# Kernel tuning notes

Hardware: AMD Instinct MI355X
Metric: run time of the kernel (lower is better)

## Reference

```python
import jax, jax.numpy as jnp
import numpy as np
from jax import lax

BN_EPS = 1e-5
C = 256


def _conv_bn_relu(x, w, gamma, beta, mean, var):
    # x: [B,C,H,W], w: [C,C,3,3]; VALID conv, stride 1, then inference BN + ReLU
    y = lax.conv_general_dilated(x, w, window_strides=(1, 1), padding='VALID',
                                 dimension_numbers=('NCHW', 'OIHW', 'NCHW'))
    scale = gamma * lax.rsqrt(var + BN_EPS)
    shift = beta - mean * scale
    y = y * scale[None, :, None, None] + shift[None, :, None, None]
    return jax.nn.relu(y)


def _xcorr_depthwise(search, kernel):
    # search: [B,C,Hs,Ws], kernel: [B,C,Hk,Wk]
    # per-(batch, channel) valid cross-correlation (groups = B*C in torch)
    c = search.shape[1]

    def one(s, k):  # s: [C,Hs,Ws], k: [C,Hk,Wk]
        return lax.conv_general_dilated(
            s[None], k[:, None], window_strides=(1, 1), padding='VALID',
            dimension_numbers=('NCHW', 'OIHW', 'NCHW'),
            feature_group_count=c)[0]

    return jax.vmap(one)(search, kernel)  # [B,C,Ho,Wo]


def setup_inputs() -> dict:
    key = jax.random.key(0)
    ks = jax.random.split(key, 8)
    B = 128
    kernel = jax.random.normal(ks[0], (B, C, 7, 7), dtype=jnp.float32)
    search = jax.random.normal(ks[1], (B, C, 31, 31), dtype=jnp.float32)
    std = np.sqrt(2.0 / (3 * 3 * C)).astype(np.float32)
    w_kernel = jax.random.normal(ks[2], (C, C, 3, 3), dtype=jnp.float32) * std
    w_search = jax.random.normal(ks[3], (C, C, 3, 3), dtype=jnp.float32) * std
    bn_k_gamma = jnp.ones((C,), jnp.float32)
    bn_k_beta = jnp.zeros((C,), jnp.float32)
    bn_k_mean = jax.random.normal(ks[4], (C,), dtype=jnp.float32) * 0.1
    bn_k_var = jax.random.uniform(ks[5], (C,), dtype=jnp.float32, minval=0.5, maxval=1.5)
    bn_s_gamma = jnp.ones((C,), jnp.float32)
    bn_s_beta = jnp.zeros((C,), jnp.float32)
    bn_s_mean = jax.random.normal(ks[6], (C,), dtype=jnp.float32) * 0.1
    bn_s_var = jax.random.uniform(ks[7], (C,), dtype=jnp.float32, minval=0.5, maxval=1.5)
    return dict(kernel=kernel, search=search,
                w_kernel=w_kernel, bn_k_gamma=bn_k_gamma, bn_k_beta=bn_k_beta,
                bn_k_mean=bn_k_mean, bn_k_var=bn_k_var,
                w_search=w_search, bn_s_gamma=bn_s_gamma, bn_s_beta=bn_s_beta,
                bn_s_mean=bn_s_mean, bn_s_var=bn_s_var)


def reference(kernel, search, w_kernel, bn_k_gamma, bn_k_beta, bn_k_mean, bn_k_var,
              w_search, bn_s_gamma, bn_s_beta, bn_s_mean, bn_s_var):
    k = _conv_bn_relu(kernel, w_kernel, bn_k_gamma, bn_k_beta, bn_k_mean, bn_k_var)  # [B,C,5,5]
    s = _conv_bn_relu(search, w_search, bn_s_gamma, bn_s_beta, bn_s_mean, bn_s_var)  # [B,C,29,29]
    return _xcorr_depthwise(s, k)  # [B,C,25,25]
```

## Files before the change

### kernel.cpp

```cpp
#include <hip/hip_runtime.h>
#include <hip/hip_bf16.h>

#define BN_EPS 1e-5f
constexpr int C = 256;

typedef __attribute__((ext_vector_type(8))) short bf16x8;
typedef __attribute__((ext_vector_type(4))) float f32x4;

static __device__ __forceinline__ unsigned short f2bf(float f) {
    __hip_bfloat16 h = __float2bfloat16(f);
    return *reinterpret_cast<unsigned short*>(&h);
}
static __device__ __forceinline__ float bf2f(unsigned short u) {
    unsigned int v = ((unsigned int)u) << 16;
    return __uint_as_float(v);
}

__global__ __launch_bounds__(256) void prep_fused(
    const float* __restrict__ wk, const float* __restrict__ bkg, const float* __restrict__ bkv,
    unsigned short* __restrict__ wkt,
    const float* __restrict__ ws, const float* __restrict__ bsg, const float* __restrict__ bsv,
    unsigned short* __restrict__ wst,
    const float* __restrict__ kin, unsigned short* __restrict__ ipk,
    int nw)
{
    __shared__ float s_t[64][65];
    const int bid = blockIdx.x;
    const int t = threadIdx.x;

    if (bid < nw) {
        const bool isk = bid < (nw >> 1);
        const int n = isk ? bid : bid - (nw >> 1);
        const float* w = isk ? wk : ws;
        const float* g = isk ? bkg : bsg;
        const float* v = isk ? bkv : bsv;
        unsigned short* wt = isk ? wkt : wst;
        const float scale = g[n] * rsqrtf(v[n] + BN_EPS);
        const float* wp = w + ((size_t)n * C + t) * 9;
#pragma unroll
        for (int k = 0; k < 9; ++k)
            wt[((size_t)k * C + n) * C + t] = f2bf(wp[k] * scale);
        return;
    }

    const int idx = bid - nw;
    const int b = idx >> 2, c0 = (idx & 3) * 64;
    constexpr int HW = 49;
    const float* ip = kin + ((size_t)b * C + c0) * HW;

#pragma unroll
    for (int it = 0; it < 4; ++it) {
        int i = t + it * 256;
        int cl = i >> 4, q = i & 15;
#pragma unroll
        for (int j = 0; j < 4; ++j) {
            int p = q * 4 + j;
            s_t[cl][p] = (p < HW) ? ip[(size_t)cl * HW + p] : 0.f;
        }
    }
    __syncthreads();

    unsigned short* op = ipk + (size_t)b * HW * C + c0;
#pragma unroll
    for (int it = 0; it < 2; ++it) {
        int i = t + it * 256;
        int pl = i >> 3, gq = i & 7;
        if (pl < HW) {
            bf16x8 pk;
#pragma unroll
            for (int u = 0; u < 8; ++u)
                pk[u] = (short)f2bf(s_t[gq * 8 + u][pl]);
            *(bf16x8*)&op[(size_t)pl * C + gq * 8] = pk;
        }
    }
}

__global__ __launch_bounds__(256) void l2_fused(
    const float* __restrict__ sin_, unsigned short* __restrict__ ips,
    const unsigned short* __restrict__ ipk, const unsigned short* __restrict__ wkt,
    const float* __restrict__ bkg, const float* __restrict__ bkb,
    const float* __restrict__ bkm, const float* __restrict__ bkv,
    float* __restrict__ kbuf, int nkc)
{
    __shared__ __align__(16) char smem[16640];
    const int bid = blockIdx.x;
    const int t = threadIdx.x;

    if (bid < nkc) {
        constexpr int WIN = 7, HW = 49, WOUT = 5, NPOS = 25;
        constexpr int BPB = 2, PPB = 32, MF = 2, NF = 2;
        constexpr int APIX = 49, LDK = 40;
        constexpr int SLOTS_B = APIX * 4, SLOTS = BPB * SLOTS_B;
        constexpr int ITERS = 2;

        short* s_a = (short*)smem;

        const int lane = t & 63, wave = t >> 6;
        const int wm = wave >> 1, wn = wave & 1;
        const int lr = lane >> 4, lc = lane & 15;

        const int n0 = (bid & 3) * 64;
        const int b0 = (bid >> 2) * 2;

        int arow[MF];
#pragma unroll
        for (int m = 0; m < MF; ++m) {
            int pm = wm * 32 + m * 16 + lc;
            int bb = pm / PPB;
            int p = pm % PPB;
            p = p < NPOS ? p : NPOS - 1;
            int y = p / WOUT, x = p % WOUT;
            arow[m] = (bb * APIX + y * WIN + x) * LDK;
        }

        f32x4 acc[MF][NF];
#pragma unroll
        for (int m = 0; m < MF; ++m)
#pragma unroll
            for (int n = 0; n < NF; ++n) acc[m][n] = f32x4{0.f, 0.f, 0.f, 0.f};

        int sbb[ITERS], spx[ITERS], ssl[ITERS];
#pragma unroll
        for (int it = 0; it < ITERS; ++it) {
            int i = t + it * 256;
            int ii = i < SLOTS ? i : 0;
            int bb = ii / SLOTS_B;
            int r = ii - bb * SLOTS_B;
            sbb[it] = bb; spx[it] = r >> 2; ssl[it] = r & 3;
        }

        const unsigned short* wb = wkt + (size_t)(n0 + wn * 32 + lc) * C + lr * 8;

#define K_LOAD(c0_)                                                            \
        _Pragma("unroll")                                                      \
        for (int it = 0; it < ITERS; ++it) {                                   \
            const unsigned short* sp =                                         \
                ipk + ((size_t)(b0 + sbb[it]) * HW + spx[it]) * C + (c0_) + ssl[it] * 8; \
            stg[it] = *(const bf16x8*)sp;                                      \
        }
#define K_WRITE()                                                              \
        _Pragma("unroll")                                                      \
        for (int it = 0; it < ITERS; ++it)                                     \
            *(bf16x8*)&s_a[(sbb[it] * APIX + spx[it]) * LDK + ssl[it] * 8] = stg[it];

        {
            bf16x8 stg[ITERS];
            K_LOAD(0)
            K_WRITE()
        }

#pragma unroll 1
        for (int ch = 0; ch < 8; ++ch) {
            const int c0 = ch * 32;
            __syncthreads();

            bf16x8 stg[ITERS];
            if (ch < 7) { K_LOAD(c0 + 32) }

            bf16x8 bcur[NF], bnxt[NF];
#pragma unroll
            for (int n = 0; n < NF; ++n)
                bnxt[n] = *(const bf16x8*)&wb[(size_t)0 * (C * C) + n * (16 * C) + c0];

#pragma unroll
            for (int tap = 0; tap < 9; ++tap) {
                const int dy = tap / 3, dx = tap % 3;
#pragma unroll
                for (int n = 0; n < NF; ++n) bcur[n] = bnxt[n];
                if (tap < 8) {
#pragma unroll
                    for (int n = 0; n < NF; ++n)
                        bnxt[n] = *(const bf16x8*)&wb[(size_t)(tap + 1) * (C * C) + n * (16 * C) + c0];
                }
                bf16x8 af[MF];
#pragma unroll
                for (int m = 0; m < MF; ++m)
                    af[m] = *(const bf16x8*)&s_a[arow[m] + (dy * WIN + dx) * LDK + lr * 8];
#pragma unroll
                for (int m = 0; m < MF; ++m)
#pragma unroll
                    for (int n = 0; n < NF; ++n)
                        acc[m][n] = __builtin_amdgcn_mfma_f32_16x16x32_bf16(
                            af[m], bcur[n], acc[m][n], 0, 0, 0);
            }

            __syncthreads();
            if (ch < 7) { K_WRITE() }
        }
#undef K_LOAD
#undef K_WRITE

#pragma unroll
        for (int n = 0; n < NF; ++n) {
            const int co = n0 + wn * 32 + n * 16 + lc;
            const float sc = bkg[co] * rsqrtf(bkv[co] + BN_EPS);
            const float bias = bkb[co] - bkm[co] * sc;
#pragma unroll
            for (int m = 0; m < MF; ++m) {
                int pm = wm * 32 + m * 16 + lr * 4;
                int bb = pm / PPB;
                int p = pm % PPB;
                int b = b0 + bb;
                f32x4 v = acc[m][n];
                float rr[4] = {fmaxf(v.x + bias, 0.f), fmaxf(v.y + bias, 0.f),
                               fmaxf(v.z + bias, 0.f), fmaxf(v.w + bias, 0.f)};
                float* op = kbuf + ((size_t)b * C + co) * 28 + p;
#pragma unroll
                for (int i = 0; i < 4; ++i)
                    if (p + i < NPOS) op[i] = rr[i];
            }
        }
        return;
    }

    {
        constexpr int HW = 961;
        float (*s_t)[65] = (float(*)[65])smem;
        const int idx = bid - nkc;
        const int px0 = (idx & 15) * 64;
        const int c0 = ((idx >> 4) & 3) * 64;
        const int b = idx >> 6;
        const float* ip = sin_ + ((size_t)b * C + c0) * HW;

#pragma unroll
        for (int it = 0; it < 4; ++it) {
            int i = t + it * 256;
            int cl = i >> 4, q = i & 15;
#pragma unroll
            for (int j = 0; j < 4; ++j) {
                int p = px0 + q * 4 + j;
                s_t[cl][q * 4 + j] = (p < HW) ? ip[(size_t)cl * HW + p] : 0.f;
            }
        }
        __syncthreads();

        unsigned short* op = ips + (size_t)b * HW * C + (size_t)px0 * C + c0;
#pragma unroll
        for (int it = 0; it < 2; ++it) {
            int i = t + it * 256;
            int pl = i >> 3, gq = i & 7;
            if (px0 + pl < HW) {
                bf16x8 pk;
#pragma unroll
                for (int u = 0; u < 8; ++u)
                    pk[u] = (short)f2bf(s_t[gq * 8 + u][pl]);
                *(bf16x8*)&op[(size_t)pl * C + gq * 8] = pk;
            }
        }
    }
}

__global__ __launch_bounds__(512, 2) void sconv_mfma(
    const unsigned short* __restrict__ in,
    const unsigned short* __restrict__ wt,
    const float* __restrict__ gamma, const float* __restrict__ beta,
    const float* __restrict__ mean, const float* __restrict__ var,
    unsigned short* __restrict__ outp)
{
    constexpr int WOUT = 29, NPOS = 841;
    constexpr int BM = 224, MF = 7, NF = 4;
    constexpr int LDK = 36;
    constexpr int ROWS = 11;
    constexpr int APIX = ROWS * 31;
    constexpr int ABUF = APIX * LDK;
    constexpr int BBUF = 256 * LDK;
    constexpr int AIT = 3;
    constexpr int BIT = 2;

    __shared__ __align__(16) short s_a[2 * ABUF];
    __shared__ __align__(16) short s_b[4 * BBUF];

    const int t = threadIdx.x;
    const int lane = t & 63, wave = t >> 6;
    const int wm = wave >> 2, wn = wave & 3;
    const int lr = lane >> 4, lc = lane & 15;

    const int p0 = blockIdx.x * BM;
    const int b  = blockIdx.y;
    const int y0 = p0 / WOUT;
    const int R  = min(ROWS, 31 - y0);
    const int npix = R * 31;

    const unsigned short* in_b = in + (size_t)b * (961 * 256);

    int arow[MF];
#pragma unroll
    for (int m = 0; m < MF; ++m) {
        int pm = wm * 112 + m * 16 + lc;
        int p = p0 + pm; p = p < NPOS ? p : NPOS - 1;
        int y = p / WOUT, x = p - y * WOUT;
        arow[m] = ((y - y0) * 31 + x) * LDK + lr * 8;
    }

    const unsigned short* aptr[AIT]; int aoff[AIT];
#pragma unroll
    for (int it = 0; it < AIT; ++it) {
        int i = t + it * 512;
        int px = i >> 2, sl = i & 3;
        px = px < npix ? px : 0;
        aptr[it] = in_b + (size_t)(y0 * 31 + px) * 256 + sl * 8;
        aoff[it] = px * LDK + sl * 8;
    }
    const unsigned short* bptr[BIT]; int boff[BIT];
#pragma unroll
    for (int it = 0; it < BIT; ++it) {
        int i = t + it * 512;
        int n = i >> 2, sl = i & 3;
        bptr[it] = wt + (size_t)n * 256 + sl * 8;
        boff[it] = n * LDK + sl * 8;
    }

    f32x4 acc[MF][NF];
#pragma unroll
    for (int m = 0; m < MF; ++m)
#pragma unroll
        for (int n = 0; n < NF; ++n) acc[m][n] = f32x4{0.f, 0.f, 0.f, 0.f};

    bf16x8 bstg0[BIT], bstg1[BIT], astg[AIT];

#pragma unroll
    for (int it = 0; it < BIT; ++it) bstg0[it] = *(const bf16x8*)(bptr[it]);
#pragma unroll
    for (int it = 0; it < BIT; ++it) bstg1[it] = *(const bf16x8*)(bptr[it] + 65536);
#pragma unroll
    for (int it = 0; it < AIT; ++it) astg[it] = *(const bf16x8*)(aptr[it]);
#pragma unroll
    for (int it = 0; it < BIT; ++it) *(bf16x8*)&s_b[boff[it]] = bstg0[it];
#pragma unroll
    for (int it = 0; it < BIT; ++it) *(bf16x8*)&s_b[BBUF + boff[it]] = bstg1[it];
#pragma unroll
    for (int it = 0; it < AIT; ++it) *(bf16x8*)&s_a[aoff[it]] = astg[it];
    __syncthreads();

#define READ_FRAGS(S, AF, BF)                                                  \
    {                                                                          \
        const int tap_ = (S) % 9;                                              \
        const int dt_ = (tap_ / 3) * 31 + (tap_ % 3);                          \
        const int ab_ = (((S) / 9) & 1) * ABUF;                                \
        const int bb_ = ((S) & 3) * BBUF;                                      \
        _Pragma("unroll")                                                      \
        for (int n = 0; n < NF; ++n)                                           \
            BF[n] = *(const bf16x8*)&s_b[bb_ + (wn * 64 + n * 16 + lc) * LDK + lr * 8]; \
        _Pragma("unroll")                                                      \
        for (int m = 0; m < MF; ++m)                                           \
            AF[m] = *(const bf16x8*)&s_a[ab_ + arow[m] + dt_ * LDK];           \
    }

#define MFMA_STEP(AF, BF)                                                      \
    _Pragma("unroll")                                                          \
    for (int m = 0; m < MF; ++m)                                               \
        _Pragma("unroll")                                                      \
        for (int n = 0; n < NF; ++n)                                           \
            acc[m][n] = __builtin_amdgcn_mfma_f32_16x16x32_bf16(               \
                AF[m], BF[n], acc[m][n], 0, 0, 0);

#pragma unroll 1
    for (int pr = 0; pr < 35; ++pr) {
        const int s0 = 2 * pr, s1 = s0 + 1;

        {
            const int cb = (s0 % 9 == 0) ? s0 / 9 : ((s1 % 9 == 0) ? s1 / 9 : -1);
            if (cb >= 0 && cb < 7) {
                const int co_ = (cb + 1) * 32;
#pragma unroll
                for (int it = 0; it < AIT; ++it)
                    astg[it] = *(const bf16x8*)(aptr[it] + co_);
            }
        }

        bf16x8 af0[MF], bf0[NF], af1[MF], bf1[NF];
        READ_FRAGS(s0, af0, bf0)
        READ_FRAGS(s1, af1, bf1)

        MFMA_STEP(af0, bf0)

        {
            const int u0 = s0 + 2, u1 = s1 + 2;
            const int t0 = u0 % 9, c0_ = (u0 / 9) * 32;
            const int t1 = u1 % 9, c1_ = (u1 / 9) * 32;
#pragma unroll
            for (int it = 0; it < BIT; ++it)
                bstg0[it] = *(const bf16x8*)(bptr[it] + (size_t)t0 * 65536 + c0_);
#pragma unroll
            for (int it = 0; it < BIT; ++it)
                bstg1[it] = *(const bf16x8*)(bptr[it] + (size_t)t1 * 65536 + c1_);
        }

        MFMA_STEP(af1, bf1)

        {
            const int w0 = ((s0 + 2) & 3) * BBUF, w1 = ((s1 + 2) & 3) * BBUF;
#pragma unroll
            for (int it = 0; it < BIT; ++it)
                *(bf16x8*)&s_b[w0 + boff[it]] = bstg0[it];
#pragma unroll
            for (int it = 0; it < BIT; ++it)
                *(bf16x8*)&s_b[w1 + boff[it]] = bstg1[it];
        }

        __builtin_amdgcn_sched_group_barrier(0x100, 11, 0);
#pragma unroll
        for (int q = 0; q < 5; ++q) {
            __builtin_amdgcn_sched_group_barrier(0x008, 3, 0);
            __builtin_amdgcn_sched_group_barrier(0x100, 1, 0);
        }
#pragma unroll
        for (int q = 0; q < 6; ++q) {
            __builtin_amdgcn_sched_group_barrier(0x008, 2, 0);
            __builtin_amdgcn_sched_group_barrier(0x100, 1, 0);
        }
        __builtin_amdgcn_sched_group_barrier(0x008, 1, 0);
        __builtin_amdgcn_sched_group_barrier(0x020, 4, 0);
        __builtin_amdgcn_sched_group_barrier(0x008, 28, 0);
        __builtin_amdgcn_sched_group_barrier(0x200, 4, 0);

        {
            const int cw = (s0 % 9 == 7) ? s0 / 9 : ((s1 % 9 == 7) ? s1 / 9 : -1);
            if (cw >= 0 && cw < 7) {
                const int dst = ((cw & 1) ^ 1) * ABUF;
#pragma unroll
                for (int it = 0; it < AIT; ++it)
                    *(bf16x8*)&s_a[dst + aoff[it]] = astg[it];
            }
        }
        __syncthreads();
    }

    {
        bf16x8 af0[MF], bf0[NF], af1[MF], bf1[NF];
        READ_FRAGS(70, af0, bf0)
        READ_FRAGS(71, af1, bf1)
        MFMA_STEP(af0, bf0)
        MFMA_STEP(af1, bf1)
    }
#undef READ_FRAGS
#undef MFMA_STEP

#pragma unroll
    for (int n = 0; n < NF; ++n) {
        const int co = wn * 64 + n * 16 + lc;
        const float sc = gamma[co] * rsqrtf(var[co] + BN_EPS);
        const float bias = beta[co] - mean[co] * sc;
#pragma unroll
        for (int m = 0; m < MF; ++m) {
            int pm = wm * 112 + m * 16 + lr * 4;
            int p = p0 + pm;
            f32x4 v = acc[m][n];
            float r0 = fmaxf(v.x + bias, 0.f);
            float r1 = fmaxf(v.y + bias, 0.f);
            float r2 = fmaxf(v.z + bias, 0.f);
            float r3 = fmaxf(v.w + bias, 0.f);
            unsigned short* op = outp + ((size_t)b * C + co) * 844 + p;
            if (p + 4 <= NPOS) {
                ushort4 pk;
                pk.x = f2bf(r0); pk.y = f2bf(r1); pk.z = f2bf(r2); pk.w = f2bf(r3);
                *(ushort4*)op = pk;
            } else {
                float rr[4] = {r0, r1, r2, r3};
#pragma unroll
                for (int i = 0; i < 4; ++i)
                    if (p + i < NPOS) op[i] = f2bf(rr[i]);
            }
        }
    }
}

__global__ __launch_bounds__(256) void xcorr_dw(
    const unsigned short* __restrict__ s, const float* __restrict__ k,
    float* __restrict__ out)
{
    const int bc0 = blockIdx.x * 2;
    const int t = threadIdx.x;

    __shared__ float s_s[2][844];
    __shared__ float s_k[2][25];

#pragma unroll
    for (int it = 0; it < 2; ++it) {
        int i = t + it * 256;
        if (i < 422) {
            int pl = i < 211 ? 0 : 1;
            int q = i - pl * 211;
            ushort4 v = *(const ushort4*)(s + (size_t)(bc0 + pl) * 844 + 4 * q);
            s_s[pl][4 * q + 0] = bf2f(v.x);
            s_s[pl][4 * q + 1] = bf2f(v.y);
            s_s[pl][4 * q + 2] = bf2f(v.z);
            s_s[pl][4 * q + 3] = bf2f(v.w);
        }
    }
    if (t < 50) s_k[t / 25][t % 25] = k[(size_t)(bc0 + t / 25) * 28 + t % 25];
    __syncthreads();

    if (t >= 250) return;
    const int ch = t / 125;
    const int r = t - ch * 125;
    const int y = r / 5;
    const int xb = (r - y * 5) * 5;

    float kk[25];
#pragma unroll
    for (int i = 0; i < 25; ++i) kk[i] = s_k[ch][i];

    float w[5][9];
#pragma unroll
    for (int dy = 0; dy < 5; ++dy)
#pragma unroll
        for (int dx = 0; dx < 9; ++dx)
            w[dy][dx] = s_s[ch][(y + dy) * 29 + xb + dx];

    float o[5] = {0.f, 0.f, 0.f, 0.f, 0.f};
#pragma unroll
    for (int dy = 0; dy < 5; ++dy)
#pragma unroll
        for (int dx = 0; dx < 5; ++dx) {
            const float kv = kk[dy * 5 + dx];
#pragma unroll
            for (int oo = 0; oo < 5; ++oo)
                o[oo] += w[dy][oo + dx] * kv;
        }

    float* op = out + (size_t)(bc0 + ch) * 625 + y * 25 + xb;
#pragma unroll
    for (int oo = 0; oo < 5; ++oo) op[oo] = o[oo];
}

extern "C" void kernel_launch(void* const* d_in, const int* in_sizes, int n_in,
                              void* d_out, int out_size, void* d_ws, size_t ws_size,
                              hipStream_t stream) {
    const float* kin = (const float*)d_in[0];
    const float* sin_ = (const float*)d_in[1];
    const float* wk = (const float*)d_in[2];
    const float* bkg = (const float*)d_in[3];
    const float* bkb = (const float*)d_in[4];
    const float* bkm = (const float*)d_in[5];
    const float* bkv = (const float*)d_in[6];
    const float* ws_ = (const float*)d_in[7];
    const float* bsg = (const float*)d_in[8];
    const float* bsb = (const float*)d_in[9];
    const float* bsm = (const float*)d_in[10];
    const float* bsv = (const float*)d_in[11];
    float* out = (float*)d_out;

    char* base = (char*)d_ws;
    unsigned short* wkt = (unsigned short*)base;
    unsigned short* wst = wkt + (size_t)9 * C * C;
    char* gbase = base + 2359296;

    const size_t perb_is = (size_t)961 * C * 2;
    const size_t perb_ik = (size_t)49 * C * 2;
    const size_t perb_sb = (size_t)844 * C * 2;
    const size_t perb_kb = (size_t)28 * C * 4;
    const size_t perb = perb_is + perb_ik + perb_sb + perb_kb;

    int G = (int)((ws_size - 2359296) / perb);
    if (G > 128) G = 128;
    G &= ~1;
    if (G < 2) G = 2;

    unsigned short* ips  = (unsigned short*)gbase;
    unsigned short* ipk  = (unsigned short*)(gbase + (size_t)G * perb_is);
    unsigned short* sbuf = (unsigned short*)(gbase + (size_t)G * (perb_is + perb_ik));
    float*          kbuf = (float*)(gbase + (size_t)G * (perb_is + perb_ik + perb_sb));

    for (int g0 = 0; g0 < 128; g0 += G) {
        const int g = (128 - g0) < G ? (128 - g0) : G;
        const int nw = (g0 == 0) ? 512 : 0;

        prep_fused<<<nw + 4 * g, 256, 0, stream>>>(
            wk, bkg, bkv, wkt, ws_, bsg, bsv, wst,
            kin + (size_t)g0 * C * 49, ipk, nw);

        const int nkc = 2 * g;
        l2_fused<<<nkc + 64 * g, 256, 0, stream>>>(
            sin_ + (size_t)g0 * C * 961, ips, ipk, wkt,
            bkg, bkb, bkm, bkv, kbuf, nkc);

        sconv_mfma<<<dim3(4, g), 512, 0, stream>>>(
            ips, wst, bsg, bsb, bsm, bsv, sbuf);

        xcorr_dw<<<(unsigned)g * (C / 2), 256, 0, stream>>>(
            sbuf, kbuf, out + (size_t)g0 * C * 625);
    }
}
```

Measured before the change: 262.2 us.

## Fuse input transpose into conv kernels and merge both convs into one launch

Removes the separate NCHW-to-NHWC bf16 transpose passes for the search and template inputs. The conv kernels now read fp32 NCHW directly, pack pairs of channels to bf16 and write them into shared memory. Both 3x3 convs go into a single mega_conv launch with block ranges split by blockIdx, and the per-group batching loop and the manual sched_group_barrier ordering are dropped. This saves a full round trip of the transposed intermediates through global memory and several launches. In exchange, the global loads inside the main MFMA loop are strided 4-byte scalar reads instead of 16-byte vectors, and the hand-tuned instruction interleaving is lost.

```diff
diff --git a/kernel.cpp b/kernel.cpp
--- a/kernel.cpp
+++ b/kernel.cpp
@@ -15,247 +15,41 @@
     unsigned int v = ((unsigned int)u) << 16;
     return __uint_as_float(v);
 }
-
-__global__ __launch_bounds__(256) void prep_fused(
+static __device__ __forceinline__ unsigned int pack_bf2(float a, float b) {
+    return (unsigned int)f2bf(a) | ((unsigned int)f2bf(b) << 16);
+}
+
+__global__ __launch_bounds__(256) void wprep_both(
     const float* __restrict__ wk, const float* __restrict__ bkg, const float* __restrict__ bkv,
     unsigned short* __restrict__ wkt,
     const float* __restrict__ ws, const float* __restrict__ bsg, const float* __restrict__ bsv,
-    unsigned short* __restrict__ wst,
-    const float* __restrict__ kin, unsigned short* __restrict__ ipk,
-    int nw)
+    unsigned short* __restrict__ wst)
 {
-    __shared__ float s_t[64][65];
-    const int bid = blockIdx.x;
-    const int t = threadIdx.x;
-
-    if (bid < nw) {
-        const bool isk = bid < (nw >> 1);
-        const int n = isk ? bid : bid - (nw >> 1);
-        const float* w = isk ? wk : ws;
-        const float* g = isk ? bkg : bsg;
-        const float* v = isk ? bkv : bsv;
-        unsigned short* wt = isk ? wkt : wst;
-        const float scale = g[n] * rsqrtf(v[n] + BN_EPS);
-        const float* wp = w + ((size_t)n * C + t) * 9;
-#pragma unroll
-        for (int k = 0; k < 9; ++k)
-            wt[((size_t)k * C + n) * C + t] = f2bf(wp[k] * scale);
-        return;
-    }
-
-    const int idx = bid - nw;
-    const int b = idx >> 2, c0 = (idx & 3) * 64;
-    constexpr int HW = 49;
-    const float* ip = kin + ((size_t)b * C + c0) * HW;
-
-#pragma unroll
-    for (int it = 0; it < 4; ++it) {
-        int i = t + it * 256;
-        int cl = i >> 4, q = i & 15;
-#pragma unroll
-        for (int j = 0; j < 4; ++j) {
-            int p = q * 4 + j;
-            s_t[cl][p] = (p < HW) ? ip[(size_t)cl * HW + p] : 0.f;
-        }
-    }
-    __syncthreads();
-
-    unsigned short* op = ipk + (size_t)b * HW * C + c0;
-#pragma unroll
-    for (int it = 0; it < 2; ++it) {
-        int i = t + it * 256;
-        int pl = i >> 3, gq = i & 7;
-        if (pl < HW) {
-            bf16x8 pk;
-#pragma unroll
-            for (int u = 0; u < 8; ++u)
-                pk[u] = (short)f2bf(s_t[gq * 8 + u][pl]);
-            *(bf16x8*)&op[(size_t)pl * C + gq * 8] = pk;
-        }
-    }
-}
-
-__global__ __launch_bounds__(256) void l2_fused(
-    const float* __restrict__ sin_, unsigned short* __restrict__ ips,
-    const unsigned short* __restrict__ ipk, const unsigned short* __restrict__ wkt,
+    const int bid = blockIdx.x, t = threadIdx.x;
+    const bool isk = bid < 256;
+    const int n = isk ? bid : bid - 256;
+    const float* w = isk ? wk : ws;
+    const float* g = isk ? bkg : bsg;
+    const float* v = isk ? bkv : bsv;
+    unsigned short* wt = isk ? wkt : wst;
+    const float scale = g[n] * rsqrtf(v[n] + BN_EPS);
+    const float* wp = w + ((size_t)n * C + t) * 9;
+#pragma unroll
+    for (int k = 0; k < 9; ++k)
+        wt[((size_t)k * C + n) * C + t] = f2bf(wp[k] * scale);
+}
+
+__global__ __launch_bounds__(512, 2) void mega_conv(
+    const float* __restrict__ sin_,
+    const float* __restrict__ kin,
+    const unsigned short* __restrict__ wst,
+    const unsigned short* __restrict__ wkt,
+    const float* __restrict__ bsg, const float* __restrict__ bsb,
+    const float* __restrict__ bsm, const float* __restrict__ bsv,
     const float* __restrict__ bkg, const float* __restrict__ bkb,
     const float* __restrict__ bkm, const float* __restrict__ bkv,
-    float* __restrict__ kbuf, int nkc)
-{
-    __shared__ __align__(16) char smem[16640];
-    const int bid = blockIdx.x;
-    const int t = threadIdx.x;
-
-    if (bid < nkc) {
-        constexpr int WIN = 7, HW = 49, WOUT = 5, NPOS = 25;
-        constexpr int BPB = 2, PPB = 32, MF = 2, NF = 2;
-        constexpr int APIX = 49, LDK = 40;
-        constexpr int SLOTS_B = APIX * 4, SLOTS = BPB * SLOTS_B;
-        constexpr int ITERS = 2;
-
-        short* s_a = (short*)smem;
-
-        const int lane = t & 63, wave = t >> 6;
-        const int wm = wave >> 1, wn = wave & 1;
-        const int lr = lane >> 4, lc = lane & 15;
-
-        const int n0 = (bid & 3) * 64;
-        const int b0 = (bid >> 2) * 2;
-
-        int arow[MF];
-#pragma unroll
-        for (int m = 0; m < MF; ++m) {
-            int pm = wm * 32 + m * 16 + lc;
-            int bb = pm / PPB;
-            int p = pm % PPB;
-            p = p < NPOS ? p : NPOS - 1;
-            int y = p / WOUT, x = p % WOUT;
-            arow[m] = (bb * APIX + y * WIN + x) * LDK;
-        }
-
-        f32x4 acc[MF][NF];
-#pragma unroll
-        for (int m = 0; m < MF; ++m)
-#pragma unroll
-            for (int n = 0; n < NF; ++n) acc[m][n] = f32x4{0.f, 0.f, 0.f, 0.f};
-
-        int sbb[ITERS], spx[ITERS], ssl[ITERS];
-#pragma unroll
-        for (int it = 0; it < ITERS; ++it) {
-            int i = t + it * 256;
-            int ii = i < SLOTS ? i : 0;
-            int bb = ii / SLOTS_B;
-            int r = ii - bb * SLOTS_B;
-            sbb[it] = bb; spx[it] = r >> 2; ssl[it] = r & 3;
-        }
-
-        const unsigned short* wb = wkt + (size_t)(n0 + wn * 32 + lc) * C + lr * 8;
-
-#define K_LOAD(c0_)                                                            \
-        _Pragma("unroll")                                                      \
-        for (int it = 0; it < ITERS; ++it) {                                   \
-            const unsigned short* sp =                                         \
-                ipk + ((size_t)(b0 + sbb[it]) * HW + spx[it]) * C + (c0_) + ssl[it] * 8; \
-            stg[it] = *(const bf16x8*)sp;                                      \
-        }
-#define K_WRITE()                                                              \
-        _Pragma("unroll")                                                      \
-        for (int it = 0; it < ITERS; ++it)                                     \
-            *(bf16x8*)&s_a[(sbb[it] * APIX + spx[it]) * LDK + ssl[it] * 8] = stg[it];
-
-        {
-            bf16x8 stg[ITERS];
-            K_LOAD(0)
-            K_WRITE()
-        }
-
-#pragma unroll 1
-        for (int ch = 0; ch < 8; ++ch) {
-            const int c0 = ch * 32;
-            __syncthreads();
-
-            bf16x8 stg[ITERS];
-            if (ch < 7) { K_LOAD(c0 + 32) }
-
-            bf16x8 bcur[NF], bnxt[NF];
-#pragma unroll
-            for (int n = 0; n < NF; ++n)
-                bnxt[n] = *(const bf16x8*)&wb[(size_t)0 * (C * C) + n * (16 * C) + c0];
-
-#pragma unroll
-            for (int tap = 0; tap < 9; ++tap) {
-                const int dy = tap / 3, dx = tap % 3;
-#pragma unroll
-                for (int n = 0; n < NF; ++n) bcur[n] = bnxt[n];
-                if (tap < 8) {
-#pragma unroll
-                    for (int n = 0; n < NF; ++n)
-                        bnxt[n] = *(const bf16x8*)&wb[(size_t)(tap + 1) * (C * C) + n * (16 * C) + c0];
-                }
-                bf16x8 af[MF];
-#pragma unroll
-                for (int m = 0; m < MF; ++m)
-                    af[m] = *(const bf16x8*)&s_a[arow[m] + (dy * WIN + dx) * LDK + lr * 8];
-#pragma unroll
-                for (int m = 0; m < MF; ++m)
-#pragma unroll
-                    for (int n = 0; n < NF; ++n)
-                        acc[m][n] = __builtin_amdgcn_mfma_f32_16x16x32_bf16(
-                            af[m], bcur[n], acc[m][n], 0, 0, 0);
-            }
-
-            __syncthreads();
-            if (ch < 7) { K_WRITE() }
-        }
-#undef K_LOAD
-#undef K_WRITE
-
-#pragma unroll
-        for (int n = 0; n < NF; ++n) {
-            const int co = n0 + wn * 32 + n * 16 + lc;
-            const float sc = bkg[co] * rsqrtf(bkv[co] + BN_EPS);
-            const float bias = bkb[co] - bkm[co] * sc;
-#pragma unroll
-            for (int m = 0; m < MF; ++m) {
-                int pm = wm * 32 + m * 16 + lr * 4;
-                int bb = pm / PPB;
-                int p = pm % PPB;
-                int b = b0 + bb;
-                f32x4 v = acc[m][n];
-                float rr[4] = {fmaxf(v.x + bias, 0.f), fmaxf(v.y + bias, 0.f),
-                               fmaxf(v.z + bias, 0.f), fmaxf(v.w + bias, 0.f)};
-                float* op = kbuf + ((size_t)b * C + co) * 28 + p;
-#pragma unroll
-                for (int i = 0; i < 4; ++i)
-                    if (p + i < NPOS) op[i] = rr[i];
-            }
-        }
-        return;
-    }
-
-    {
-        constexpr int HW = 961;
-        float (*s_t)[65] = (float(*)[65])smem;
-        const int idx = bid - nkc;
-        const int px0 = (idx & 15) * 64;
-        const int c0 = ((idx >> 4) & 3) * 64;
-        const int b = idx >> 6;
-        const float* ip = sin_ + ((size_t)b * C + c0) * HW;
-
-#pragma unroll
-        for (int it = 0; it < 4; ++it) {
-            int i = t + it * 256;
-            int cl = i >> 4, q = i & 15;
-#pragma unroll
-            for (int j = 0; j < 4; ++j) {
-                int p = px0 + q * 4 + j;
-                s_t[cl][q * 4 + j] = (p < HW) ? ip[(size_t)cl * HW + p] : 0.f;
-            }
-        }
-        __syncthreads();
-
-        unsigned short* op = ips + (size_t)b * HW * C + (size_t)px0 * C + c0;
-#pragma unroll
-        for (int it = 0; it < 2; ++it) {
-            int i = t + it * 256;
-            int pl = i >> 3, gq = i & 7;
-            if (px0 + pl < HW) {
-                bf16x8 pk;
-#pragma unroll
-                for (int u = 0; u < 8; ++u)
-                    pk[u] = (short)f2bf(s_t[gq * 8 + u][pl]);
-                *(bf16x8*)&op[(size_t)pl * C + gq * 8] = pk;
-            }
-        }
-    }
-}
-
-__global__ __launch_bounds__(512, 2) void sconv_mfma(
-    const unsigned short* __restrict__ in,
-    const unsigned short* __restrict__ wt,
-    const float* __restrict__ gamma, const float* __restrict__ beta,
-    const float* __restrict__ mean, const float* __restrict__ var,
-    unsigned short* __restrict__ outp)
+    unsigned short* __restrict__ sbuf,
+    float* __restrict__ kbuf)
 {
     constexpr int WOUT = 29, NPOS = 841;
     constexpr int BM = 224, MF = 7, NF = 4;
@@ -264,24 +58,139 @@
     constexpr int APIX = ROWS * 31;
     constexpr int ABUF = APIX * LDK;
     constexpr int BBUF = 256 * LDK;
-    constexpr int AIT = 3;
     constexpr int BIT = 2;
 
     __shared__ __align__(16) short s_a[2 * ABUF];
     __shared__ __align__(16) short s_b[4 * BBUF];
 
+    const int bid = blockIdx.x;
     const int t = threadIdx.x;
     const int lane = t & 63, wave = t >> 6;
+    const int lr = lane >> 4, lc = lane & 15;
+
+    if (bid >= 512) {
+        constexpr int KW = 7, KHW = 49, KWOUT = 5, KNPOS = 25;
+        constexpr int KMF = 2, KNF = 2;
+        const int kb = bid - 512;
+        const int n0 = (kb & 1) * 128;
+        const int b0 = (kb >> 1) * 2;
+        const int wm = wave >> 2, wn = wave & 3;
+
+        short* ka = s_a;
+
+        int arow[KMF];
+#pragma unroll
+        for (int m = 0; m < KMF; ++m) {
+            int p = m * 16 + lc;
+            p = p < KNPOS ? p : KNPOS - 1;
+            int y = p / KWOUT, x = p - y * KWOUT;
+            arow[m] = ((wm * KHW) + y * KW + x) * LDK + lr * 8;
+        }
+
+        f32x4 acc[KMF][KNF];
+#pragma unroll
+        for (int m = 0; m < KMF; ++m)
+#pragma unroll
+            for (int n = 0; n < KNF; ++n) acc[m][n] = f32x4{0.f, 0.f, 0.f, 0.f};
+
+        const bool kval = lane < KHW;
+        int sbb[4], scq[4];
+#pragma unroll
+        for (int j = 0; j < 4; ++j) {
+            int idx = wave * 4 + j;
+            sbb[j] = idx >> 4; scq[j] = (idx & 15) * 2;
+        }
+        const float* kbase = kin + (size_t)b0 * C * KHW + lane;
+
+        float k0s[4], k1s[4];
+#define KA_LOAD(c0_)                                                           \
+        _Pragma("unroll")                                                      \
+        for (int j = 0; j < 4; ++j) {                                          \
+            if (kval) {                                                        \
+                const float* p_ = kbase + ((size_t)sbb[j] * C + (c0_) + scq[j]) * KHW; \
+                k0s[j] = p_[0]; k1s[j] = p_[KHW];                              \
+            }                                                                  \
+        }
+#define KA_WRITE()                                                             \
+        _Pragma("unroll")                                                      \
+        for (int j = 0; j < 4; ++j) {                                          \
+            if (kval)                                                          \
+                *(unsigned int*)&ka[(sbb[j] * KHW + lane) * LDK + scq[j]] =    \
+                    pack_bf2(k0s[j], k1s[j]);                                  \
+        }
+
+        const unsigned short* wb = wkt + (size_t)(n0 + wn * 32 + lc) * C + lr * 8;
+
+        KA_LOAD(0)
+        KA_WRITE()
+
+#pragma unroll 1
+        for (int ch = 0; ch < 8; ++ch) {
+            const int c0 = ch * 32;
+            __syncthreads();
+
+            if (ch < 7) { KA_LOAD(c0 + 32) }
+
+            bf16x8 bcur[KNF], bnxt[KNF];
+#pragma unroll
+            for (int n = 0; n < KNF; ++n)
+                bnxt[n] = *(const bf16x8*)&wb[(size_t)0 + n * (16 * C) + c0];
+
+#pragma unroll
+            for (int tap = 0; tap < 9; ++tap) {
+                const int dy = tap / 3, dx = tap % 3;
+#pragma unroll
+                for (int n = 0; n < KNF; ++n) bcur[n] = bnxt[n];
+                if (tap < 8) {
+#pragma unroll
+                    for (int n = 0; n < KNF; ++n)
+                        bnxt[n] = *(const bf16x8*)&wb[(size_t)(tap + 1) * (C * C) + n * (16 * C) + c0];
+                }
+                bf16x8 af[KMF];
+#pragma unroll
+                for (int m = 0; m < KMF; ++m)
+                    af[m] = *(const bf16x8*)&ka[arow[m] + (dy * KW + dx) * LDK];
+#pragma unroll
+                for (int m = 0; m < KMF; ++m)
+#pragma unroll
+                    for (int n = 0; n < KNF; ++n)
+                        acc[m][n] = __builtin_amdgcn_mfma_f32_16x16x32_bf16(
+                            af[m], bcur[n], acc[m][n], 0, 0, 0);
+            }
+
+            __syncthreads();
+            if (ch < 7) { KA_WRITE() }
+        }
+#undef KA_LOAD
+#undef KA_WRITE
+
+#pragma unroll
+        for (int n = 0; n < KNF; ++n) {
+            const int co = n0 + wn * 32 + n * 16 + lc;
+            const float sc = bkg[co] * rsqrtf(bkv[co] + BN_EPS);
+            const float bias = bkb[co] - bkm[co] * sc;
+#pragma unroll
+            for (int m = 0; m < KMF; ++m) {
+                int p = m * 16 + lr * 4;
+                int b = b0 + wm;
+                f32x4 v = acc[m][n];
+                float rr[4] = {fmaxf(v.x + bias, 0.f), fmaxf(v.y + bias, 0.f),
+                               fmaxf(v.z + bias, 0.f), fmaxf(v.w + bias, 0.f)};
+                float* op = kbuf + ((size_t)b * C + co) * 28 + p;
+#pragma unroll
+                for (int i = 0; i < 4; ++i)
+                    if (p + i < KNPOS) op[i] = rr[i];
+            }
+        }
+        return;
+    }
+
     const int wm = wave >> 2, wn = wave & 3;
-    const int lr = lane >> 4, lc = lane & 15;
-
-    const int p0 = blockIdx.x * BM;
-    const int b  = blockIdx.y;
+    const int p0 = (bid & 3) * BM;
+    const int b  = bid >> 2;
     const int y0 = p0 / WOUT;
     const int R  = min(ROWS, 31 - y0);
     const int npix = R * 31;
-
-    const unsigned short* in_b = in + (size_t)b * (961 * 256);
 
     int arow[MF];
 #pragma unroll
@@ -292,21 +201,44 @@
         arow[m] = ((y - y0) * 31 + x) * LDK + lr * 8;
     }
 
-    const unsigned short* aptr[AIT]; int aoff[AIT];
-#pragma unroll
-    for (int it = 0; it < AIT; ++it) {
-        int i = t + it * 512;
-        int px = i >> 2, sl = i & 3;
-        px = px < npix ? px : 0;
-        aptr[it] = in_b + (size_t)(y0 * 31 + px) * 256 + sl * 8;
-        aoff[it] = px * LDK + sl * 8;
-    }
+    const float* abase = sin_ + (size_t)b * C * 961 + y0 * 31 + lane;
+    bool segv[6];
+    int dstq[2];
+#pragma unroll
+    for (int seg = 0; seg < 6; ++seg) segv[seg] = (seg * 64 + lane) < npix;
+#pragma unroll
+    for (int q = 0; q < 2; ++q) dstq[q] = 2 * (wave + q * 8);
+
+    float a0s[12], a1s[12];
+#define SA_LOAD(c0_)                                                           \
+    _Pragma("unroll")                                                          \
+    for (int q = 0; q < 2; ++q) {                                              \
+        const size_t cq_ = (size_t)((c0_) + dstq[q]) * 961;                    \
+        _Pragma("unroll")                                                      \
+        for (int seg = 0; seg < 6; ++seg) {                                    \
+            if (segv[seg]) {                                                   \
+                a0s[q * 6 + seg] = abase[cq_ + seg * 64];                      \
+                a1s[q * 6 + seg] = abase[cq_ + 961 + seg * 64];                \
+            }                                                                  \
+        }                                                                      \
+    }
+#define SA_WRITE(dst_)                                                         \
+    _Pragma("unroll")                                                          \
+    for (int q = 0; q < 2; ++q) {                                              \
+        _Pragma("unroll")                                                      \
+        for (int seg = 0; seg < 6; ++seg) {                                    \
+            if (segv[seg])                                                     \
+                *(unsigned int*)&s_a[(dst_) + (seg * 64 + lane) * LDK + dstq[q]] = \
+                    pack_bf2(a0s[q * 6 + seg], a1s[q * 6 + seg]);              \
+        }                                                                      \
+    }
+
     const unsigned short* bptr[BIT]; int boff[BIT];
 #pragma unroll
     for (int it = 0; it < BIT; ++it) {
         int i = t + it * 512;
         int n = i >> 2, sl = i & 3;
-        bptr[it] = wt + (size_t)n * 256 + sl * 8;
+        bptr[it] = wst + (size_t)n * 256 + sl * 8;
         boff[it] = n * LDK + sl * 8;
     }
 
@@ -316,20 +248,18 @@
 #pragma unroll
         for (int n = 0; n < NF; ++n) acc[m][n] = f32x4{0.f, 0.f, 0.f, 0.f};
 
-    bf16x8 bstg0[BIT], bstg1[BIT], astg[AIT];
-
+    bf16x8 bstg0[BIT], bstg1[BIT];
+
+    SA_LOAD(0)
 #pragma unroll
     for (int it = 0; it < BIT; ++it) bstg0[it] = *(const bf16x8*)(bptr[it]);
 #pragma unroll
     for (int it = 0; it < BIT; ++it) bstg1[it] = *(const bf16x8*)(bptr[it] + 65536);
-#pragma unroll
-    for (int it = 0; it < AIT; ++it) astg[it] = *(const bf16x8*)(aptr[it]);
+    SA_WRITE(0)
 #pragma unroll
     for (int it = 0; it < BIT; ++it) *(bf16x8*)&s_b[boff[it]] = bstg0[it];
 #pragma unroll
     for (int it = 0; it < BIT; ++it) *(bf16x8*)&s_b[BBUF + boff[it]] = bstg1[it];
-#pragma unroll
-    for (int it = 0; it < AIT; ++it) *(bf16x8*)&s_a[aoff[it]] = astg[it];
     __syncthreads();
 
 #define READ_FRAGS(S, AF, BF)                                                  \
@@ -361,10 +291,8 @@
         {
             const int cb = (s0 % 9 == 0) ? s0 / 9 : ((s1 % 9 == 0) ? s1 / 9 : -1);
             if (cb >= 0 && cb < 7) {
-                const int co_ = (cb + 1) * 32;
-#pragma unroll
-                for (int it = 0; it < AIT; ++it)
-                    astg[it] = *(const bf16x8*)(aptr[it] + co_);
+                const int cn = (cb + 1) * 32;
+                SA_LOAD(cn)
             }
         }
 
@@ -398,29 +326,11 @@
                 *(bf16x8*)&s_b[w1 + boff[it]] = bstg1[it];
         }
 
-        __builtin_amdgcn_sched_group_barrier(0x100, 11, 0);
-#pragma unroll
-        for (int q = 0; q < 5; ++q) {
-            __builtin_amdgcn_sched_group_barrier(0x008, 3, 0);
-            __builtin_amdgcn_sched_group_barrier(0x100, 1, 0);
-        }
-#pragma unroll
-        for (int q = 0; q < 6; ++q) {
-            __builtin_amdgcn_sched_group_barrier(0x008, 2, 0);
-            __builtin_amdgcn_sched_group_barrier(0x100, 1, 0);
-        }
-        __builtin_amdgcn_sched_group_barrier(0x008, 1, 0);
-        __builtin_amdgcn_sched_group_barrier(0x020, 4, 0);
-        __builtin_amdgcn_sched_group_barrier(0x008, 28, 0);
-        __builtin_amdgcn_sched_group_barrier(0x200, 4, 0);
-
         {
             const int cw = (s0 % 9 == 7) ? s0 / 9 : ((s1 % 9 == 7) ? s1 / 9 : -1);
             if (cw >= 0 && cw < 7) {
                 const int dst = ((cw & 1) ^ 1) * ABUF;
-#pragma unroll
-                for (int it = 0; it < AIT; ++it)
-                    *(bf16x8*)&s_a[dst + aoff[it]] = astg[it];
+                SA_WRITE(dst)
             }
         }
         __syncthreads();
@@ -435,12 +345,14 @@
     }
 #undef READ_FRAGS
 #undef MFMA_STEP
+#undef SA_LOAD
+#undef SA_WRITE
 
 #pragma unroll
     for (int n = 0; n < NF; ++n) {
         const int co = wn * 64 + n * 16 + lc;
-        const float sc = gamma[co] * rsqrtf(var[co] + BN_EPS);
-        const float bias = beta[co] - mean[co] * sc;
+        const float sc = bsg[co] * rsqrtf(bsv[co] + BN_EPS);
+        const float bias = bsb[co] - bsm[co] * sc;
 #pragma unroll
         for (int m = 0; m < MF; ++m) {
             int pm = wm * 112 + m * 16 + lr * 4;
@@ -450,7 +362,7 @@
             float r1 = fmaxf(v.y + bias, 0.f);
             float r2 = fmaxf(v.z + bias, 0.f);
             float r3 = fmaxf(v.w + bias, 0.f);
-            unsigned short* op = outp + ((size_t)b * C + co) * 844 + p;
+            unsigned short* op = sbuf + ((size_t)b * C + co) * 844 + p;
             if (p + 4 <= NPOS) {
                 ushort4 pk;
                 pk.x = f2bf(r0); pk.y = f2bf(r1); pk.z = f2bf(r2); pk.w = f2bf(r3);
@@ -544,41 +456,15 @@
     char* base = (char*)d_ws;
     unsigned short* wkt = (unsigned short*)base;
     unsigned short* wst = wkt + (size_t)9 * C * C;
-    char* gbase = base + 2359296;
-
-    const size_t perb_is = (size_t)961 * C * 2;
-    const size_t perb_ik = (size_t)49 * C * 2;
-    const size_t perb_sb = (size_t)844 * C * 2;
-    const size_t perb_kb = (size_t)28 * C * 4;
-    const size_t perb = perb_is + perb_ik + perb_sb + perb_kb;
-
-    int G = (int)((ws_size - 2359296) / perb);
-    if (G > 128) G = 128;
-    G &= ~1;
-    if (G < 2) G = 2;
-
-    unsigned short* ips  = (unsigned short*)gbase;
-    unsigned short* ipk  = (unsigned short*)(gbase + (size_t)G * perb_is);
-    unsigned short* sbuf = (unsigned short*)(gbase + (size_t)G * (perb_is + perb_ik));
-    float*          kbuf = (float*)(gbase + (size_t)G * (perb_is + perb_ik + perb_sb));
-
-    for (int g0 = 0; g0 < 128; g0 += G) {
-        const int g = (128 - g0) < G ? (128 - g0) : G;
-        const int nw = (g0 == 0) ? 512 : 0;
-
-        prep_fused<<<nw + 4 * g, 256, 0, stream>>>(
-            wk, bkg, bkv, wkt, ws_, bsg, bsv, wst,
-            kin + (size_t)g0 * C * 49, ipk, nw);
-
-        const int nkc = 2 * g;
-        l2_fused<<<nkc + 64 * g, 256, 0, stream>>>(
-            sin_ + (size_t)g0 * C * 961, ips, ipk, wkt,
-            bkg, bkb, bkm, bkv, kbuf, nkc);
-
-        sconv_mfma<<<dim3(4, g), 512, 0, stream>>>(
-            ips, wst, bsg, bsb, bsm, bsv, sbuf);
-
-        xcorr_dw<<<(unsigned)g * (C / 2), 256, 0, stream>>>(
-            sbuf, kbuf, out + (size_t)g0 * C * 625);
-    }
-}
+    unsigned short* sbuf = (unsigned short*)(base + 2359296);
+    float* kbuf = (float*)(base + 2359296 + 55312384);
+
+    wprep_both<<<512, 256, 0, stream>>>(wk, bkg, bkv, wkt, ws_, bsg, bsv, wst);
+
+    mega_conv<<<640, 512, 0, stream>>>(
+        sin_, kin, wst, wkt,
+        bsg, bsb, bsm, bsv, bkg, bkb, bkm, bkv,
+        sbuf, kbuf);
+
+    xcorr_dw<<<128 * (C / 2), 256, 0, stream>>>(sbuf, kbuf, out);
+}
```

Result: faster. 224.2 us (-14.5%).
